# Optimization experiments

Hardware: AMD Instinct MI355X
Metric: run time of the kernel (lower is better)

Reference implementation:

```python
import jax, jax.numpy as jnp
import numpy as np

N, E, D, B = 50000, 800000, 64, 64
NEXP, NC, EDIM, PDIM = 4, 10, 4, 100


def setup_inputs() -> dict:
    key = jax.random.key(0)
    ks = jax.random.split(key, 24)
    s = lambda f: 1.0 / np.sqrt(f)
    inp = {
        'x': jax.random.normal(ks[0], (N, D), jnp.float32),
        'edge_index': jax.random.randint(ks[1], (2, E), 0, N, jnp.int32),
        'edge_attr': jax.random.normal(ks[2], (E, EDIM), jnp.float32),
        'batch': jnp.sort(jax.random.randint(ks[3], (N,), 0, B, jnp.int32)),
        'ldxb_flag': jax.random.normal(ks[4], (B,), jnp.float32),
        # layer 1 params
        'w_edge1': jax.random.normal(ks[5], (D, EDIM)) * s(EDIM),
        'b_edge1': jnp.zeros((D,), jnp.float32),
        'w_ih1': jax.random.normal(ks[6], (3 * D, D)) * s(D),
        'w_hh1': jax.random.normal(ks[7], (3 * D, D)) * s(D),
        'b_ih1': jnp.zeros((3 * D,), jnp.float32),
        'b_hh1': jnp.zeros((3 * D,), jnp.float32),
        # layer 2 params
        'w_edge2': jax.random.normal(ks[8], (D, EDIM)) * s(EDIM),
        'b_edge2': jnp.zeros((D,), jnp.float32),
        'w_ih2': jax.random.normal(ks[9], (3 * D, D)) * s(D),
        'w_hh2': jax.random.normal(ks[10], (3 * D, D)) * s(D),
        'b_ih2': jnp.zeros((3 * D,), jnp.float32),
        'b_hh2': jnp.zeros((3 * D,), jnp.float32),
        # MoE
        'gate_w': jax.random.normal(ks[11], (NEXP, D)) * s(D),
        'gate_b': jnp.zeros((NEXP,), jnp.float32),
        'exp_w': jax.random.normal(ks[12], (NEXP, D, D)) * s(D),
        'exp_b': jnp.zeros((NEXP, D), jnp.float32),
        # heads
        'proj_w': jax.random.normal(ks[13], (PDIM, 1)),
        'proj_b': jnp.zeros((PDIM,), jnp.float32),
        'fc_w': jax.random.normal(ks[14], (NC, D + PDIM)) * s(D + PDIM),
        'fc_b': jnp.zeros((NC,), jnp.float32),
    }
    return inp


def _ggnn_layer(x, src, dst, eemb, w_ih, w_hh, b_ih, b_hh):
    # gather + scatter-add message passing (self-loops already in src/dst/eemb)
    msg = x[src] + eemb                       # [E+N, D]
    m = jnp.zeros_like(x).at[dst].add(msg)    # [N, D]
    # GRUCell(m, x): x is the hidden state
    gi = m @ w_ih.T + b_ih
    gh = x @ w_hh.T + b_hh
    i_r, i_z, i_n = jnp.split(gi, 3, axis=1)
    h_r, h_z, h_n = jnp.split(gh, 3, axis=1)
    r = jax.nn.sigmoid(i_r + h_r)
    z = jax.nn.sigmoid(i_z + h_z)
    n = jnp.tanh(i_n + r * h_n)
    return (1.0 - z) * n + z * x


def reference(x, edge_index, edge_attr, batch, ldxb_flag,
              w_edge1, b_edge1, w_ih1, w_hh1, b_ih1, b_hh1,
              w_edge2, b_edge2, w_ih2, w_hh2, b_ih2, b_hh2,
              gate_w, gate_b, exp_w, exp_b, proj_w, proj_b, fc_w, fc_b):
    n = x.shape[0]
    loop = jnp.arange(n, dtype=edge_index.dtype)
    src = jnp.concatenate([edge_index[0], loop])
    dst = jnp.concatenate([edge_index[1], loop])
    ea = jnp.concatenate([edge_attr, jnp.zeros((n, edge_attr.shape[1]), edge_attr.dtype)], axis=0)

    h = _ggnn_layer(x, src, dst, ea @ w_edge1.T + b_edge1, w_ih1, w_hh1, b_ih1, b_hh1)
    h = jax.nn.relu(h)
    h = _ggnn_layer(h, src, dst, ea @ w_edge2.T + b_edge2, w_ih2, w_hh2, b_ih2, b_hh2)
    h = jax.nn.relu(h)

    # soft MoE combine
    gw = jax.nn.softmax(h @ gate_w.T + gate_b, axis=1)            # [N, NEXP]
    eo = jax.nn.relu(jnp.einsum('nd,ehd->neh', h, exp_w) + exp_b)  # [N, NEXP, D]
    h = jnp.einsum('ne,neh->nh', gw, eo)                           # [N, D]

    # global mean pool per graph
    sums = jax.ops.segment_sum(h, batch, num_segments=B)
    cnts = jax.ops.segment_sum(jnp.ones((n,), h.dtype), batch, num_segments=B)
    graph_emb = sums / jnp.maximum(cnts, 1.0)[:, None]             # [B, D]

    flag = ldxb_flag[:, None] @ proj_w.T + proj_b                  # [B, 100]
    logits = jnp.concatenate([flag, graph_emb], axis=1) @ fc_w.T + fc_b
    return (graph_emb, graph_emb, logits)
```

## Files before the change

kernel.cpp:

```cpp
#include <hip/hip_runtime.h>
#include <hip/hip_fp16.h>
#include <stdint.h>


#define SUBCAP 8
#define OVF_MAX 32768
#define PS 16

typedef __bf16 bf16x8 __attribute__((ext_vector_type(8)));
typedef float floatx4 __attribute__((ext_vector_type(4)));
typedef unsigned short us8 __attribute__((ext_vector_type(8)));

__device__ __forceinline__ unsigned short f2bf(float f){
  union { float f; unsigned u; } c; c.f = f;
  unsigned r = c.u + 0x7FFFu + ((c.u >> 16) & 1u);
  return (unsigned short)(r >> 16);
}
__device__ __forceinline__ float bf2f(unsigned short u){
  union { unsigned u; float f; } c; c.u = ((unsigned)u) << 16; return c.f;
}
__device__ __forceinline__ unsigned short f2h(float f){
  return __half_as_ushort(__float2half(f));
}
__device__ __forceinline__ float h2f(unsigned short u){
  return __half2float(__ushort_as_half(u));
}
__device__ __forceinline__ float sigm(float x){ return 1.f/(1.f + __expf(-x)); }

__global__ void k_init(const float* __restrict__ s0, const float* __restrict__ s1,
                       const float* __restrict__ s2, const float* __restrict__ s3,
                       const float* __restrict__ s4, const float* __restrict__ s5,
                       unsigned short* __restrict__ dst,
                       int* __restrict__ cur, int* __restrict__ ovfcnt, int N8,
                       const float* __restrict__ xin, unsigned short* __restrict__ x16,
                       int nTot){
  int i = blockIdx.x*blockDim.x + threadIdx.x;
  if (i < N8) cur[i] = 0;
  if (i == 0){ ovfcnt[0] = 0; }
  int base = i*8;
  if (base < nTot){
    const float4* xp = (const float4*)(xin + base);
    float4 a = xp[0], b = xp[1];
    us8 t;
    t[0]=f2h(a.x); t[1]=f2h(a.y); t[2]=f2h(a.z); t[3]=f2h(a.w);
    t[4]=f2h(b.x); t[5]=f2h(b.y); t[6]=f2h(b.z); t[7]=f2h(b.w);
    *(us8*)(x16 + base) = t;
  }
  if (i >= 65792) return;
  const float* s; int off;
  if      (i < 12288){ s = s0; off = i; }
  else if (i < 24576){ s = s1; off = i - 12288; }
  else if (i < 36864){ s = s2; off = i - 24576; }
  else if (i < 49152){ s = s3; off = i - 36864; }
  else if (i < 49408){ s = s4; off = i - 49152; }
  else               { s = s5; off = i - 49408; }
  dst[i] = f2bf(s[off]);
}

__global__ void k_bucket(const int* __restrict__ ei, const float* __restrict__ ea,
                         int* __restrict__ cur, int4* __restrict__ bkt,
                         int* __restrict__ ovfcnt, int* __restrict__ ovf,
                         int E, int N){
  unsigned xcc;
  asm volatile("s_getreg_b32 %0, hwreg(HW_REG_XCC_ID)" : "=s"(xcc));
  int sub = (int)(xcc & 7u);
  int base = blockIdx.x*512;
#pragma unroll
  for (int half = 0; half < 2; ++half){
    int e = base + half*256 + threadIdx.x;
    if (e >= E) continue;
    int s = ei[e];
    int d = ei[E + e];
    size_t sb = (size_t)sub*N + d;
    int pos = __hip_atomic_fetch_add(&cur[sb], 1, __ATOMIC_RELAXED,
                                     __HIP_MEMORY_SCOPE_WORKGROUP);
    if (pos < SUBCAP){
      float4 v = *(const float4*)(ea + (size_t)e*4);
      int4 p;
      p.x = s;
      p.y = (int)(((unsigned)f2bf(v.y) << 16) | (unsigned)f2bf(v.x));
      p.z = (int)(((unsigned)f2bf(v.w) << 16) | (unsigned)f2bf(v.z));
      p.w = 0;
      bkt[sb*SUBCAP + pos] = p;
    } else {
      int o = atomicAdd(ovfcnt, 1);
      if (o < OVF_MAX) ovf[o] = e;
    }
  }
}

__global__ void __launch_bounds__(256) k_gather(
    const int* __restrict__ cur, const int4* __restrict__ bkt,
    const float* __restrict__ xin, const unsigned short* __restrict__ x16,
    const float* __restrict__ w_edge, const float* __restrict__ b_edge,
    float* __restrict__ m, int N){
  int n = (int)(((long long)blockIdx.x*blockDim.x + threadIdx.x) >> 6);
  if (n >= N) return;
  int d = threadIdx.x & 63;
  int sub = d >> 3, k = d & 7;
  size_t sb = (size_t)sub*N + n;
  int myc = cur[sb];
  int contrib = (k == 0) ? myc : 0;
#pragma unroll
  for (int off = 1; off < 64; off <<= 1) contrib += __shfl_xor(contrib, off);
  int degAll = contrib;

  bool valid = k < min(myc, SUBCAP);
  int src = 0;
  float esx = 0.f, esy = 0.f, esz = 0.f, esw = 0.f;
  if (valid){
    int4 p = bkt[sb*SUBCAP + k];
    src = p.x;
    esx = bf2f((unsigned short)(p.y & 0xffff));
    esy = bf2f((unsigned short)(((unsigned)p.y) >> 16));
    esz = bf2f((unsigned short)(p.z & 0xffff));
    esw = bf2f((unsigned short)(((unsigned)p.z) >> 16));
  }

  float4 wv = *(const float4*)(w_edge + d*4);
  float acc = xin[(size_t)n*64 + d] + (float)(degAll + 1) * b_edge[d];

  unsigned long long mm = __ballot(valid);
  while (mm){
    float a0=0.f,a1=0.f,a2=0.f,a3=0.f,a4=0.f,a5=0.f,a6=0.f,a7=0.f;
    {
      int l0 = (int)__builtin_ctzll(mm); mm &= mm - 1;
      a0 = h2f(x16[(size_t)__shfl(src, l0)*64 + d]);
      if (mm){
        int l1 = (int)__builtin_ctzll(mm); mm &= mm - 1;
        a1 = h2f(x16[(size_t)__shfl(src, l1)*64 + d]);
        if (mm){
          int l2 = (int)__builtin_ctzll(mm); mm &= mm - 1;
          a2 = h2f(x16[(size_t)__shfl(src, l2)*64 + d]);
          if (mm){
            int l3 = (int)__builtin_ctzll(mm); mm &= mm - 1;
            a3 = h2f(x16[(size_t)__shfl(src, l3)*64 + d]);
            if (mm){
              int l4 = (int)__builtin_ctzll(mm); mm &= mm - 1;
              a4 = h2f(x16[(size_t)__shfl(src, l4)*64 + d]);
              if (mm){
                int l5 = (int)__builtin_ctzll(mm); mm &= mm - 1;
                a5 = h2f(x16[(size_t)__shfl(src, l5)*64 + d]);
                if (mm){
                  int l6 = (int)__builtin_ctzll(mm); mm &= mm - 1;
                  a6 = h2f(x16[(size_t)__shfl(src, l6)*64 + d]);
                  if (mm){
                    int l7 = (int)__builtin_ctzll(mm); mm &= mm - 1;
                    a7 = h2f(x16[(size_t)__shfl(src, l7)*64 + d]);
                  }
                }
              }
            }
          }
        }
      }
    }
    acc += ((a0 + a1) + (a2 + a3)) + ((a4 + a5) + (a6 + a7));
  }

#pragma unroll
  for (int off = 1; off < 64; off <<= 1){
    esx += __shfl_xor(esx, off);
    esy += __shfl_xor(esy, off);
    esz += __shfl_xor(esz, off);
    esw += __shfl_xor(esw, off);
  }
  acc += esx*wv.x + esy*wv.y + esz*wv.z + esw*wv.w;
  m[(size_t)n*64 + d] = acc;
}

__global__ void k_ovf(const int* __restrict__ ei, const float* __restrict__ ea,
                      const float* __restrict__ xin, const float* __restrict__ w_edge,
                      const int* __restrict__ ovf, const int* __restrict__ ovfcnt,
                      float* __restrict__ m, int E){
  int cnt = *ovfcnt; if (cnt > OVF_MAX) cnt = OVF_MAX;
  int nwaves = (gridDim.x * blockDim.x) >> 6;
  int wid = (int)((blockIdx.x*blockDim.x + threadIdx.x) >> 6);
  int d = threadIdx.x & 63;
  for (int k = wid; k < cnt; k += nwaves){
    int e = ovf[k];
    int s = ei[e], dst = ei[E + e];
    float4 v  = *(const float4*)(ea + (size_t)e*4);
    float4 wv = *(const float4*)(w_edge + d*4);
    float msg = xin[(size_t)s*64 + d] + v.x*wv.x + v.y*wv.y + v.z*wv.z + v.w*wv.w;
    atomicAdd(&m[(size_t)dst*64 + d], msg);
  }
}

__global__ void __launch_bounds__(256) k_gru(
    const float* __restrict__ m, const float* x,
    const unsigned short* __restrict__ wih, const unsigned short* __restrict__ whh,
    const float* __restrict__ b_ih, const float* __restrict__ b_hh,
    float* out, unsigned short* h16out, int tiles, int N){
  int tile = blockIdx.x;
  if (tile >= tiles) return;
  int j    = threadIdx.x >> 6;
  int lane = threadIdx.x & 63;
  int col = lane & 15, quad = lane >> 4;
  int na = tile*16 + col; if (na > N-1) na = N-1;

  bf16x8 am[2], ax[2];
#pragma unroll
  for (int ks = 0; ks < 2; ++ks){
    int kb = ks*32 + quad*8;
    const float4* mp = (const float4*)(m + (size_t)na*64 + kb);
    float4 lo = mp[0], hi = mp[1];
    us8 tm;
    tm[0]=f2bf(lo.x); tm[1]=f2bf(lo.y); tm[2]=f2bf(lo.z); tm[3]=f2bf(lo.w);
    tm[4]=f2bf(hi.x); tm[5]=f2bf(hi.y); tm[6]=f2bf(hi.z); tm[7]=f2bf(hi.w);
    am[ks] = __builtin_bit_cast(bf16x8, tm);
    const float4* xp = (const float4*)(x + (size_t)na*64 + kb);
    float4 xlo = xp[0], xhi = xp[1];
    us8 tx;
    tx[0]=f2bf(xlo.x); tx[1]=f2bf(xlo.y); tx[2]=f2bf(xlo.z); tx[3]=f2bf(xlo.w);
    tx[4]=f2bf(xhi.x); tx[5]=f2bf(xhi.y); tx[6]=f2bf(xhi.z); tx[7]=f2bf(xhi.w);
    ax[ks] = __builtin_bit_cast(bf16x8, tx);
  }
  __syncthreads();

  floatx4 ai[3], ah[3];
#pragma unroll
  for (int g = 0; g < 3; ++g){ ai[g] = (floatx4)0.f; ah[g] = (floatx4)0.f; }
#pragma unroll
  for (int g = 0; g < 3; ++g){
    int r = (g*4 + j)*16 + col;
#pragma unroll
    for (int ks = 0; ks < 2; ++ks){
      int kb = ks*32 + quad*8;
      bf16x8 bi = __builtin_bit_cast(bf16x8, *(const us8*)(wih + (size_t)r*64 + kb));
      ai[g] = __builtin_amdgcn_mfma_f32_16x16x32_bf16(am[ks], bi, ai[g], 0,0,0);
      bf16x8 bh = __builtin_bit_cast(bf16x8, *(const us8*)(whh + (size_t)r*64 + kb));
      ah[g] = __builtin_amdgcn_mfma_f32_16x16x32_bf16(ax[ks], bh, ah[g], 0,0,0);
    }
  }

  int d = j*16 + col;
  float bir = b_ih[d],      bhr = b_hh[d];
  float biz = b_ih[64+d],   bhz = b_hh[64+d];
  float bin = b_ih[128+d],  bhn = b_hh[128+d];
#pragma unroll
  for (int rg = 0; rg < 4; ++rg){
    int node = tile*16 + quad*4 + rg;
    if (node >= N) continue;
    float rr = sigm(ai[0][rg] + bir + ah[0][rg] + bhr);
    float zz = sigm(ai[1][rg] + biz + ah[1][rg] + bhz);
    float nn = tanhf(ai[2][rg] + bin + rr*(ah[2][rg] + bhn));
    float xv = x[(size_t)node*64 + d];
    float hv = fmaxf((1.f - zz)*nn + zz*xv, 0.f);
    out[(size_t)node*64 + d] = hv;
    if (h16out) h16out[(size_t)node*64 + d] = f2h(hv);
  }
}

__global__ void __launch_bounds__(256) k_moe(
    const float* __restrict__ h,
    const unsigned short* __restrict__ gate_w, const float* __restrict__ gate_b,
    const unsigned short* __restrict__ exp_w,  const float* __restrict__ exp_b,
    float* __restrict__ v_out, int tiles, int N){
  __shared__ float gsm[16][4];
  __shared__ float vsm[4][16][65];
  int tile = blockIdx.x;
  if (tile >= tiles) return;
  int e    = threadIdx.x >> 6;
  int lane = threadIdx.x & 63;
  int col = lane & 15, quad = lane >> 4;
  int na = tile*16 + col; if (na > N-1) na = N-1;

  bf16x8 a[2];
#pragma unroll
  for (int ks=0; ks<2; ++ks){
    int kb = ks*32 + quad*8;
    const float4* hp = (const float4*)(h + (size_t)na*64 + kb);
    float4 lo = hp[0], hi = hp[1];
    us8 th;
    th[0]=f2bf(lo.x); th[1]=f2bf(lo.y); th[2]=f2bf(lo.z); th[3]=f2bf(lo.w);
    th[4]=f2bf(hi.x); th[5]=f2bf(hi.y); th[6]=f2bf(hi.z); th[7]=f2bf(hi.w);
    a[ks] = __builtin_bit_cast(bf16x8, th);
  }

  if (e == 0){
    floatx4 accg = (floatx4)0.f;
#pragma unroll
    for (int ks=0; ks<2; ++ks){
      int kb = ks*32 + quad*8;
      us8 braw = {0,0,0,0,0,0,0,0};
      if (col < 4) braw = *(const us8*)(gate_w + col*64 + kb);
      accg = __builtin_amdgcn_mfma_f32_16x16x32_bf16(a[ks], __builtin_bit_cast(bf16x8, braw), accg, 0,0,0);
    }
    if (col < 4){
      float gb = gate_b[col];
#pragma unroll
      for (int rg=0;rg<4;++rg) gsm[quad*4+rg][col] = accg[rg] + gb;
    }
  }

  floatx4 acc[4];
#pragma unroll
  for (int nt=0;nt<4;++nt) acc[nt] = (floatx4)0.f;
#pragma unroll
  for (int nt=0;nt<4;++nt)
#pragma unroll
    for (int ks=0;ks<2;++ks){
      int kb = ks*32 + quad*8;
      bf16x8 b = __builtin_bit_cast(bf16x8,
          *(const us8*)(exp_w + ((size_t)e*64 + nt*16 + col)*64 + kb));
      acc[nt] = __builtin_amdgcn_mfma_f32_16x16x32_bf16(a[ks], b, acc[nt], 0,0,0);
    }
  __syncthreads();

#pragma unroll
  for (int rg=0; rg<4; ++rg){
    int nrow = quad*4 + rg;
    float g0=gsm[nrow][0], g1=gsm[nrow][1], g2=gsm[nrow][2], g3=gsm[nrow][3];
    float mx = fmaxf(fmaxf(g0,g1), fmaxf(g2,g3));
    float e0=__expf(g0-mx), e1=__expf(g1-mx), e2=__expf(g2-mx), e3=__expf(g3-mx);
    float we = ((e==0)?e0:(e==1)?e1:(e==2)?e2:e3) / (e0+e1+e2+e3);
#pragma unroll
    for (int nt=0;nt<4;++nt){
      int o = nt*16 + col;
      vsm[e][nrow][o] = we * fmaxf(acc[nt][rg] + exp_b[e*64 + o], 0.f);
    }
  }
  __syncthreads();

  for (int idx = threadIdx.x; idx < 1024; idx += 256){
    int nrow = idx >> 6, o = idx & 63;
    int node = tile*16 + nrow;
    if (node < N)
      v_out[(size_t)node*64 + o] = vsm[0][nrow][o] + vsm[1][nrow][o]
                                 + vsm[2][nrow][o] + vsm[3][nrow][o];
  }
}

__device__ __forceinline__ int lower_bound_i(const int* __restrict__ a, int n, int key){
  int lo = 0, hi = n;
  while (lo < hi){ int mid = (lo + hi) >> 1; if (a[mid] < key) lo = mid + 1; else hi = mid; }
  return lo;
}

__global__ void __launch_bounds__(256) k_pool(
    const float* __restrict__ v, const int* __restrict__ batch, int N,
    float* __restrict__ partial){
  __shared__ float red[4][64];
  int g = blockIdx.x / PS, s = blockIdx.x % PS;
  int t = threadIdx.x, d = t & 63, r = t >> 6;
  int start = lower_bound_i(batch, N, g);
  int end   = lower_bound_i(batch, N, g + 1);
  int len = end - start;
  int per = (len + PS - 1) / PS;
  int s0 = start + s*per;
  int s1 = s0 + per; if (s1 > end) s1 = end;
  float acc = 0.f;
  for (int i = s0 + r; i < s1; i += 4)
    acc += v[(size_t)i*64 + d];
  red[r][d] = acc;
  __syncthreads();
  if (r == 0)
    partial[(size_t)blockIdx.x*64 + d] = red[0][d] + red[1][d] + red[2][d] + red[3][d];
}

__global__ void __launch_bounds__(64) k_head(
    const float* __restrict__ partial, const int* __restrict__ batch, int N, int B,
    const float* __restrict__ ldxb,
    const float* __restrict__ proj_w, const float* __restrict__ proj_b,
    const float* __restrict__ fc_w, const float* __restrict__ fc_b,
    float* __restrict__ out){
  __shared__ float ges[64];
  int b = blockIdx.x, d = threadIdx.x;
  int start = lower_bound_i(batch, N, b);
  int end   = lower_bound_i(batch, N, b + 1);
  float sum = 0.f;
#pragma unroll
  for (int s = 0; s < PS; ++s)
    sum += partial[((size_t)b*PS + s)*64 + d];
  float ge = sum / fmaxf((float)(end - start), 1.f);
  ges[d] = ge;
  out[(size_t)b*64 + d]                = ge;
  out[(size_t)B*64 + (size_t)b*64 + d] = ge;
  __syncthreads();
  if (d < 10){
    float acc = fc_b[d];
    float fl = ldxb[b];
    const float* fr = fc_w + d*164;
    for (int p = 0; p < 100; ++p) acc += (fl*proj_w[p] + proj_b[p]) * fr[p];
    for (int dd = 0; dd < 64; ++dd) acc += ges[dd]*fr[100 + dd];
    out[(size_t)B*128 + (size_t)b*10 + d] = acc;
  }
}

extern "C" void kernel_launch(void* const* d_in, const int* in_sizes, int n_in,
                              void* d_out, int out_size, void* d_ws, size_t ws_size,
                              hipStream_t stream){
  const float* x      = (const float*)d_in[0];
  const int*   ei     = (const int*)d_in[1];
  const float* ea     = (const float*)d_in[2];
  const int*   batch  = (const int*)d_in[3];
  const float* ldxb   = (const float*)d_in[4];
  const float* w_edge1= (const float*)d_in[5];
  const float* b_edge1= (const float*)d_in[6];
  const float* w_ih1  = (const float*)d_in[7];
  const float* w_hh1  = (const float*)d_in[8];
  const float* b_ih1  = (const float*)d_in[9];
  const float* b_hh1  = (const float*)d_in[10];
  const float* w_edge2= (const float*)d_in[11];
  const float* b_edge2= (const float*)d_in[12];
  const float* w_ih2  = (const float*)d_in[13];
  const float* w_hh2  = (const float*)d_in[14];
  const float* b_ih2  = (const float*)d_in[15];
  const float* b_hh2  = (const float*)d_in[16];
  const float* gate_w = (const float*)d_in[17];
  const float* gate_b = (const float*)d_in[18];
  const float* exp_w  = (const float*)d_in[19];
  const float* exp_b  = (const float*)d_in[20];
  const float* proj_w = (const float*)d_in[21];
  const float* proj_b = (const float*)d_in[22];
  const float* fc_w   = (const float*)d_in[23];
  const float* fc_b   = (const float*)d_in[24];
  float* out = (float*)d_out;

  int N = in_sizes[0] / 64;
  int E = in_sizes[1] / 2;
  int B = in_sizes[4];
  int tiles = (N + 15) / 16;
  int nTot = N * 64;

  float*   m       = (float*)d_ws;
  float*   h       = m + (size_t)nTot;
  int4*    bkt     = (int4*)(h + (size_t)nTot);
  int*     cur     = (int*)(bkt + (size_t)nTot);
  int*     ovfcnt  = cur + (size_t)N*8;
  int*     ovf     = ovfcnt + 4;
  unsigned short* wbf = (unsigned short*)(ovf + OVF_MAX);
  float*   partial = (float*)(wbf + 65792);
  unsigned short* x16 = (unsigned short*)(partial + (size_t)B*PS*64);
  unsigned short* h16 = x16 + (size_t)nTot;
  unsigned short* wih1bf = wbf;
  unsigned short* whh1bf = wbf + 12288;
  unsigned short* wih2bf = wbf + 24576;
  unsigned short* whh2bf = wbf + 36864;
  unsigned short* gatebf = wbf + 49152;
  unsigned short* expbf  = wbf + 49408;

  dim3 blk(256);
  int edgeBlocks = (E + 511)/512;
  int nodeWaveBlocks = (N + 3)/4;
  int N8 = N*8;
  int initThreads = N8 > 65792 ? N8 : 65792;
  if (nTot/8 > initThreads) initThreads = nTot/8;
  int initBlocks = (initThreads + 255)/256;

  k_init<<<initBlocks, blk, 0, stream>>>(w_ih1, w_hh1, w_ih2, w_hh2, gate_w, exp_w,
                                         wbf, cur, ovfcnt, N8, x, x16, nTot);
  k_bucket<<<edgeBlocks, blk, 0, stream>>>(ei, ea, cur, bkt, ovfcnt, ovf, E, N);
  k_gather<<<nodeWaveBlocks, blk, 0, stream>>>(cur, bkt, x, x16, w_edge1, b_edge1, m, N);
  k_ovf<<<8, blk, 0, stream>>>(ei, ea, x, w_edge1, ovf, ovfcnt, m, E);
  k_gru<<<tiles, blk, 0, stream>>>(m, x, wih1bf, whh1bf, b_ih1, b_hh1, h, h16, tiles, N);
  k_gather<<<nodeWaveBlocks, blk, 0, stream>>>(cur, bkt, h, h16, w_edge2, b_edge2, m, N);
  k_ovf<<<8, blk, 0, stream>>>(ei, ea, h, w_edge2, ovf, ovfcnt, m, E);
  k_gru<<<tiles, blk, 0, stream>>>(m, h, wih2bf, whh2bf, b_ih2, b_hh2, h, (unsigned short*)nullptr, tiles, N);
  k_moe<<<tiles, blk, 0, stream>>>(h, gatebf, gate_b, expbf, exp_b, m, tiles, N);
  k_pool<<<B*PS, blk, 0, stream>>>(m, batch, N, partial);
  k_head<<<B, 64, 0, stream>>>(partial, batch, N, B, ldxb, proj_w, proj_b, fc_w, fc_b, out);
}
```

Baseline: 353.9 us.

## Fuse gather, overflow fix-up, GRU and MoE into per-tile kernels

Measured after the change: 349.8 us. About the same (-1.1%).

```diff
diff --git a/kernel.cpp b/kernel.cpp
--- a/kernel.cpp
+++ b/kernel.cpp
@@ -89,64 +89,70 @@
   }
 }
 
-__global__ void __launch_bounds__(256) k_gather(
+__device__ __forceinline__ void gather4_ovf(
     const int* __restrict__ cur, const int4* __restrict__ bkt,
     const float* __restrict__ xin, const unsigned short* __restrict__ x16,
     const float* __restrict__ w_edge, const float* __restrict__ b_edge,
-    float* __restrict__ m, int N){
-  int n = (int)(((long long)blockIdx.x*blockDim.x + threadIdx.x) >> 6);
-  if (n >= N) return;
-  int d = threadIdx.x & 63;
+    const int* __restrict__ ei, const float* __restrict__ ea,
+    const int* __restrict__ ovf, int cnt, int E,
+    float (*mt)[68], int tile, int w, int lane, int N){
+  int d = lane;
   int sub = d >> 3, k = d & 7;
-  size_t sb = (size_t)sub*N + n;
-  int myc = cur[sb];
-  int contrib = (k == 0) ? myc : 0;
-#pragma unroll
-  for (int off = 1; off < 64; off <<= 1) contrib += __shfl_xor(contrib, off);
-  int degAll = contrib;
-
-  bool valid = k < min(myc, SUBCAP);
-  int src = 0;
-  float esx = 0.f, esy = 0.f, esz = 0.f, esw = 0.f;
-  if (valid){
-    int4 p = bkt[sb*SUBCAP + k];
-    src = p.x;
-    esx = bf2f((unsigned short)(p.y & 0xffff));
-    esy = bf2f((unsigned short)(((unsigned)p.y) >> 16));
-    esz = bf2f((unsigned short)(p.z & 0xffff));
-    esw = bf2f((unsigned short)(((unsigned)p.z) >> 16));
-  }
-
   float4 wv = *(const float4*)(w_edge + d*4);
-  float acc = xin[(size_t)n*64 + d] + (float)(degAll + 1) * b_edge[d];
-
-  unsigned long long mm = __ballot(valid);
-  while (mm){
-    float a0=0.f,a1=0.f,a2=0.f,a3=0.f,a4=0.f,a5=0.f,a6=0.f,a7=0.f;
-    {
-      int l0 = (int)__builtin_ctzll(mm); mm &= mm - 1;
-      a0 = h2f(x16[(size_t)__shfl(src, l0)*64 + d]);
-      if (mm){
-        int l1 = (int)__builtin_ctzll(mm); mm &= mm - 1;
-        a1 = h2f(x16[(size_t)__shfl(src, l1)*64 + d]);
+  float be = b_edge[d];
+#pragma unroll
+  for (int nl = 0; nl < 4; ++nl){
+    int row = w*4 + nl;
+    int n = tile*16 + row;
+    if (n >= N){ mt[row][d] = 0.f; continue; }
+    size_t sb = (size_t)sub*N + n;
+    int myc = cur[sb];
+    int contrib = (k == 0) ? myc : 0;
+#pragma unroll
+    for (int off = 1; off < 64; off <<= 1) contrib += __shfl_xor(contrib, off);
+    int degAll = contrib;
+
+    bool valid = k < min(myc, SUBCAP);
+    int src = 0;
+    float esx = 0.f, esy = 0.f, esz = 0.f, esw = 0.f;
+    if (valid){
+      int4 p = bkt[sb*SUBCAP + k];
+      src = p.x;
+      esx = bf2f((unsigned short)(p.y & 0xffff));
+      esy = bf2f((unsigned short)(((unsigned)p.y) >> 16));
+      esz = bf2f((unsigned short)(p.z & 0xffff));
+      esw = bf2f((unsigned short)(((unsigned)p.z) >> 16));
+    }
+    float acc = xin[(size_t)n*64 + d] + (float)(degAll + 1) * be;
+
+    unsigned long long mm = __ballot(valid);
+    while (mm){
+      float a0=0.f,a1=0.f,a2=0.f,a3=0.f,a4=0.f,a5=0.f,a6=0.f,a7=0.f;
+      {
+        int l0 = (int)__builtin_ctzll(mm); mm &= mm - 1;
+        a0 = h2f(x16[(size_t)__shfl(src, l0)*64 + d]);
         if (mm){
-          int l2 = (int)__builtin_ctzll(mm); mm &= mm - 1;
-          a2 = h2f(x16[(size_t)__shfl(src, l2)*64 + d]);
+          int l1 = (int)__builtin_ctzll(mm); mm &= mm - 1;
+          a1 = h2f(x16[(size_t)__shfl(src, l1)*64 + d]);
           if (mm){
-            int l3 = (int)__builtin_ctzll(mm); mm &= mm - 1;
-            a3 = h2f(x16[(size_t)__shfl(src, l3)*64 + d]);
+            int l2 = (int)__builtin_ctzll(mm); mm &= mm - 1;
+            a2 = h2f(x16[(size_t)__shfl(src, l2)*64 + d]);
             if (mm){
-              int l4 = (int)__builtin_ctzll(mm); mm &= mm - 1;
-              a4 = h2f(x16[(size_t)__shfl(src, l4)*64 + d]);
+              int l3 = (int)__builtin_ctzll(mm); mm &= mm - 1;
+              a3 = h2f(x16[(size_t)__shfl(src, l3)*64 + d]);
               if (mm){
-                int l5 = (int)__builtin_ctzll(mm); mm &= mm - 1;
-                a5 = h2f(x16[(size_t)__shfl(src, l5)*64 + d]);
+                int l4 = (int)__builtin_ctzll(mm); mm &= mm - 1;
+                a4 = h2f(x16[(size_t)__shfl(src, l4)*64 + d]);
                 if (mm){
-                  int l6 = (int)__builtin_ctzll(mm); mm &= mm - 1;
-                  a6 = h2f(x16[(size_t)__shfl(src, l6)*64 + d]);
+                  int l5 = (int)__builtin_ctzll(mm); mm &= mm - 1;
+                  a5 = h2f(x16[(size_t)__shfl(src, l5)*64 + d]);
                   if (mm){
-                    int l7 = (int)__builtin_ctzll(mm); mm &= mm - 1;
-                    a7 = h2f(x16[(size_t)__shfl(src, l7)*64 + d]);
+                    int l6 = (int)__builtin_ctzll(mm); mm &= mm - 1;
+                    a6 = h2f(x16[(size_t)__shfl(src, l6)*64 + d]);
+                    if (mm){
+                      int l7 = (int)__builtin_ctzll(mm); mm &= mm - 1;
+                      a7 = h2f(x16[(size_t)__shfl(src, l7)*64 + d]);
+                    }
                   }
                 }
               }
@@ -154,57 +160,50 @@
           }
         }
       }
-    }
-    acc += ((a0 + a1) + (a2 + a3)) + ((a4 + a5) + (a6 + a7));
-  }
-
-#pragma unroll
-  for (int off = 1; off < 64; off <<= 1){
-    esx += __shfl_xor(esx, off);
-    esy += __shfl_xor(esy, off);
-    esz += __shfl_xor(esz, off);
-    esw += __shfl_xor(esw, off);
-  }
-  acc += esx*wv.x + esy*wv.y + esz*wv.z + esw*wv.w;
-  m[(size_t)n*64 + d] = acc;
-}
-
-__global__ void k_ovf(const int* __restrict__ ei, const float* __restrict__ ea,
-                      const float* __restrict__ xin, const float* __restrict__ w_edge,
-                      const int* __restrict__ ovf, const int* __restrict__ ovfcnt,
-                      float* __restrict__ m, int E){
-  int cnt = *ovfcnt; if (cnt > OVF_MAX) cnt = OVF_MAX;
-  int nwaves = (gridDim.x * blockDim.x) >> 6;
-  int wid = (int)((blockIdx.x*blockDim.x + threadIdx.x) >> 6);
-  int d = threadIdx.x & 63;
-  for (int k = wid; k < cnt; k += nwaves){
-    int e = ovf[k];
-    int s = ei[e], dst = ei[E + e];
-    float4 v  = *(const float4*)(ea + (size_t)e*4);
-    float4 wv = *(const float4*)(w_edge + d*4);
-    float msg = xin[(size_t)s*64 + d] + v.x*wv.x + v.y*wv.y + v.z*wv.z + v.w*wv.w;
-    atomicAdd(&m[(size_t)dst*64 + d], msg);
-  }
-}
-
-__global__ void __launch_bounds__(256) k_gru(
-    const float* __restrict__ m, const float* x,
+      acc += ((a0 + a1) + (a2 + a3)) + ((a4 + a5) + (a6 + a7));
+    }
+#pragma unroll
+    for (int off = 1; off < 64; off <<= 1){
+      esx += __shfl_xor(esx, off);
+      esy += __shfl_xor(esy, off);
+      esz += __shfl_xor(esz, off);
+      esw += __shfl_xor(esw, off);
+    }
+    acc += esx*wv.x + esy*wv.y + esz*wv.z + esw*wv.w;
+    mt[row][d] = acc;
+  }
+  int lo = tile*16;
+  for (int base = 0; base < cnt; base += 64){
+    int idx = base + lane;
+    int eid = (idx < cnt) ? ovf[idx] : -1;
+    int dst = (eid >= 0) ? ei[(size_t)E + eid] : -1;
+    int rel = dst - lo;
+    bool hit = (eid >= 0) && (rel >= 0) && (rel < 16) && ((rel >> 2) == w);
+    unsigned long long hm = __ballot(hit);
+    while (hm){
+      int l = (int)__builtin_ctzll(hm); hm &= hm - 1;
+      int e2 = __shfl(eid, l);
+      int r2 = __shfl(rel, l);
+      int s2 = ei[e2];
+      float4 v = *(const float4*)(ea + (size_t)e2*4);
+      float addv = xin[(size_t)s2*64 + d] + v.x*wv.x + v.y*wv.y + v.z*wv.z + v.w*wv.w;
+      mt[r2][d] += addv;
+    }
+  }
+}
+
+__device__ __forceinline__ void gru3(
+    const float (*mt)[68], const float* __restrict__ x,
     const unsigned short* __restrict__ wih, const unsigned short* __restrict__ whh,
-    const float* __restrict__ b_ih, const float* __restrict__ b_hh,
-    float* out, unsigned short* h16out, int tiles, int N){
-  int tile = blockIdx.x;
-  if (tile >= tiles) return;
-  int j    = threadIdx.x >> 6;
-  int lane = threadIdx.x & 63;
-  int col = lane & 15, quad = lane >> 4;
+    int tile, int j, int col, int quad, int N,
+    floatx4* ai, floatx4* ah){
   int na = tile*16 + col; if (na > N-1) na = N-1;
-
   bf16x8 am[2], ax[2];
 #pragma unroll
   for (int ks = 0; ks < 2; ++ks){
     int kb = ks*32 + quad*8;
-    const float4* mp = (const float4*)(m + (size_t)na*64 + kb);
-    float4 lo = mp[0], hi = mp[1];
+    const float* mrow = &mt[col][kb];
+    float4 lo = *(const float4*)mrow, hi = *(const float4*)(mrow + 4);
     us8 tm;
     tm[0]=f2bf(lo.x); tm[1]=f2bf(lo.y); tm[2]=f2bf(lo.z); tm[3]=f2bf(lo.w);
     tm[4]=f2bf(hi.x); tm[5]=f2bf(hi.y); tm[6]=f2bf(hi.z); tm[7]=f2bf(hi.w);
@@ -216,9 +215,6 @@
     tx[4]=f2bf(xhi.x); tx[5]=f2bf(xhi.y); tx[6]=f2bf(xhi.z); tx[7]=f2bf(xhi.w);
     ax[ks] = __builtin_bit_cast(bf16x8, tx);
   }
-  __syncthreads();
-
-  floatx4 ai[3], ah[3];
 #pragma unroll
   for (int g = 0; g < 3; ++g){ ai[g] = (floatx4)0.f; ah[g] = (floatx4)0.f; }
 #pragma unroll
@@ -233,11 +229,34 @@
       ah[g] = __builtin_amdgcn_mfma_f32_16x16x32_bf16(ax[ks], bh, ah[g], 0,0,0);
     }
   }
-
-  int d = j*16 + col;
-  float bir = b_ih[d],      bhr = b_hh[d];
-  float biz = b_ih[64+d],   bhz = b_hh[64+d];
-  float bin = b_ih[128+d],  bhn = b_hh[128+d];
+}
+
+__global__ void __launch_bounds__(256) k_fused1(
+    const int* __restrict__ cur, const int4* __restrict__ bkt,
+    const float* __restrict__ x, const unsigned short* __restrict__ x16,
+    const float* __restrict__ w_edge, const float* __restrict__ b_edge,
+    const int* __restrict__ ei, const float* __restrict__ ea,
+    const int* __restrict__ ovf, const int* __restrict__ ovfcnt, int E,
+    const unsigned short* __restrict__ wih, const unsigned short* __restrict__ whh,
+    const float* __restrict__ b_ih, const float* __restrict__ b_hh,
+    float* __restrict__ hout, unsigned short* __restrict__ h16out,
+    int tiles, int N){
+  __shared__ __align__(16) float mt[16][68];
+  int tile = blockIdx.x; if (tile >= tiles) return;
+  int w = threadIdx.x >> 6, lane = threadIdx.x & 63;
+  int cnt = *ovfcnt; if (cnt > OVF_MAX) cnt = OVF_MAX;
+  gather4_ovf(cur, bkt, x, x16, w_edge, b_edge, ei, ea, ovf, cnt, E,
+              mt, tile, w, lane, N);
+  __syncthreads();
+
+  int col = lane & 15, quad = lane >> 4, j = w;
+  floatx4 ai[3], ah[3];
+  gru3(mt, x, wih, whh, tile, j, col, quad, N, ai, ah);
+
+  int dd = j*16 + col;
+  float bir = b_ih[dd],      bhr = b_hh[dd];
+  float biz = b_ih[64+dd],   bhz = b_hh[64+dd];
+  float bin = b_ih[128+dd],  bhn = b_hh[128+dd];
 #pragma unroll
   for (int rg = 0; rg < 4; ++rg){
     int node = tile*16 + quad*4 + rg;
@@ -245,80 +264,106 @@
     float rr = sigm(ai[0][rg] + bir + ah[0][rg] + bhr);
     float zz = sigm(ai[1][rg] + biz + ah[1][rg] + bhz);
     float nn = tanhf(ai[2][rg] + bin + rr*(ah[2][rg] + bhn));
-    float xv = x[(size_t)node*64 + d];
+    float xv = x[(size_t)node*64 + dd];
     float hv = fmaxf((1.f - zz)*nn + zz*xv, 0.f);
-    out[(size_t)node*64 + d] = hv;
-    if (h16out) h16out[(size_t)node*64 + d] = f2h(hv);
-  }
-}
-
-__global__ void __launch_bounds__(256) k_moe(
-    const float* __restrict__ h,
+    hout[(size_t)node*64 + dd] = hv;
+    h16out[(size_t)node*64 + dd] = f2h(hv);
+  }
+}
+
+__global__ void __launch_bounds__(256) k_fused2(
+    const int* __restrict__ cur, const int4* __restrict__ bkt,
+    const float* __restrict__ h, const unsigned short* __restrict__ h16,
+    const float* __restrict__ w_edge, const float* __restrict__ b_edge,
+    const int* __restrict__ ei, const float* __restrict__ ea,
+    const int* __restrict__ ovf, const int* __restrict__ ovfcnt, int E,
+    const unsigned short* __restrict__ wih, const unsigned short* __restrict__ whh,
+    const float* __restrict__ b_ih, const float* __restrict__ b_hh,
     const unsigned short* __restrict__ gate_w, const float* __restrict__ gate_b,
     const unsigned short* __restrict__ exp_w,  const float* __restrict__ exp_b,
     float* __restrict__ v_out, int tiles, int N){
+  __shared__ __align__(16) float mt[16][68];
+  __shared__ __align__(16) unsigned short ht16s[1024];
   __shared__ float gsm[16][4];
   __shared__ float vsm[4][16][65];
-  int tile = blockIdx.x;
-  if (tile >= tiles) return;
-  int e    = threadIdx.x >> 6;
-  int lane = threadIdx.x & 63;
-  int col = lane & 15, quad = lane >> 4;
-  int na = tile*16 + col; if (na > N-1) na = N-1;
-
-  bf16x8 a[2];
-#pragma unroll
-  for (int ks=0; ks<2; ++ks){
-    int kb = ks*32 + quad*8;
-    const float4* hp = (const float4*)(h + (size_t)na*64 + kb);
-    float4 lo = hp[0], hi = hp[1];
-    us8 th;
-    th[0]=f2bf(lo.x); th[1]=f2bf(lo.y); th[2]=f2bf(lo.z); th[3]=f2bf(lo.w);
-    th[4]=f2bf(hi.x); th[5]=f2bf(hi.y); th[6]=f2bf(hi.z); th[7]=f2bf(hi.w);
-    a[ks] = __builtin_bit_cast(bf16x8, th);
-  }
-
-  if (e == 0){
+  int tile = blockIdx.x; if (tile >= tiles) return;
+  int w = threadIdx.x >> 6, lane = threadIdx.x & 63;
+  int cnt = *ovfcnt; if (cnt > OVF_MAX) cnt = OVF_MAX;
+  gather4_ovf(cur, bkt, h, h16, w_edge, b_edge, ei, ea, ovf, cnt, E,
+              mt, tile, w, lane, N);
+  __syncthreads();
+
+  int col = lane & 15, quad = lane >> 4, j = w;
+  floatx4 ai[3], ah[3];
+  gru3(mt, h, wih, whh, tile, j, col, quad, N, ai, ah);
+
+  int dd = j*16 + col;
+  {
+    float bir = b_ih[dd],      bhr = b_hh[dd];
+    float biz = b_ih[64+dd],   bhz = b_hh[64+dd];
+    float bin = b_ih[128+dd],  bhn = b_hh[128+dd];
+#pragma unroll
+    for (int rg = 0; rg < 4; ++rg){
+      int nloc = quad*4 + rg;
+      int node = tile*16 + nloc;
+      int na2 = node < N ? node : N-1;
+      float rr = sigm(ai[0][rg] + bir + ah[0][rg] + bhr);
+      float zz = sigm(ai[1][rg] + biz + ah[1][rg] + bhz);
+      float nn = tanhf(ai[2][rg] + bin + rr*(ah[2][rg] + bhn));
+      float xv = h[(size_t)na2*64 + dd];
+      float hv = fmaxf((1.f - zz)*nn + zz*xv, 0.f);
+      int addr = (nloc*128 + dd*2) ^ ((nloc & 7) << 4);
+      *(unsigned short*)((char*)ht16s + addr) = f2bf(hv);
+    }
+  }
+  __syncthreads();
+
+  bf16x8 a2[2];
+#pragma unroll
+  for (int ks = 0; ks < 2; ++ks){
+    int badd = (col*128 + ks*64 + quad*16) ^ ((col & 7) << 4);
+    a2[ks] = __builtin_bit_cast(bf16x8, *(const us8*)((const char*)ht16s + badd));
+  }
+  if (j == 0){
     floatx4 accg = (floatx4)0.f;
 #pragma unroll
-    for (int ks=0; ks<2; ++ks){
+    for (int ks = 0; ks < 2; ++ks){
       int kb = ks*32 + quad*8;
       us8 braw = {0,0,0,0,0,0,0,0};
       if (col < 4) braw = *(const us8*)(gate_w + col*64 + kb);
-      accg = __builtin_amdgcn_mfma_f32_16x16x32_bf16(a[ks], __builtin_bit_cast(bf16x8, braw), accg, 0,0,0);
+      accg = __builtin_amdgcn_mfma_f32_16x16x32_bf16(a2[ks], __builtin_bit_cast(bf16x8, braw), accg, 0,0,0);
     }
     if (col < 4){
       float gb = gate_b[col];
 #pragma unroll
-      for (int rg=0;rg<4;++rg) gsm[quad*4+rg][col] = accg[rg] + gb;
-    }
-  }
-
-  floatx4 acc[4];
-#pragma unroll
-  for (int nt=0;nt<4;++nt) acc[nt] = (floatx4)0.f;
-#pragma unroll
-  for (int nt=0;nt<4;++nt)
-#pragma unroll
-    for (int ks=0;ks<2;++ks){
+      for (int rg = 0; rg < 4; ++rg) gsm[quad*4+rg][col] = accg[rg] + gb;
+    }
+  }
+  floatx4 acc2[4];
+#pragma unroll
+  for (int nt = 0; nt < 4; ++nt) acc2[nt] = (floatx4)0.f;
+#pragma unroll
+  for (int nt = 0; nt < 4; ++nt)
+#pragma unroll
+    for (int ks = 0; ks < 2; ++ks){
       int kb = ks*32 + quad*8;
       bf16x8 b = __builtin_bit_cast(bf16x8,
-          *(const us8*)(exp_w + ((size_t)e*64 + nt*16 + col)*64 + kb));
-      acc[nt] = __builtin_amdgcn_mfma_f32_16x16x32_bf16(a[ks], b, acc[nt], 0,0,0);
-    }
-  __syncthreads();
-
-#pragma unroll
-  for (int rg=0; rg<4; ++rg){
+          *(const us8*)(exp_w + ((size_t)j*64 + nt*16 + col)*64 + kb));
+      acc2[nt] = __builtin_amdgcn_mfma_f32_16x16x32_bf16(a2[ks], b, acc2[nt], 0,0,0);
+    }
+  __syncthreads();
+
+#pragma unroll
+  for (int rg = 0; rg < 4; ++rg){
     int nrow = quad*4 + rg;
     float g0=gsm[nrow][0], g1=gsm[nrow][1], g2=gsm[nrow][2], g3=gsm[nrow][3];
     float mx = fmaxf(fmaxf(g0,g1), fmaxf(g2,g3));
     float e0=__expf(g0-mx), e1=__expf(g1-mx), e2=__expf(g2-mx), e3=__expf(g3-mx);
-    float we = ((e==0)?e0:(e==1)?e1:(e==2)?e2:e3) / (e0+e1+e2+e3);
-#pragma unroll
-    for (int nt=0;nt<4;++nt){
+    float we = ((j==0)?e0:(j==1)?e1:(j==2)?e2:e3) / (e0+e1+e2+e3);
+#pragma unroll
+    for (int nt = 0; nt < 4; ++nt){
       int o = nt*16 + col;
-      vsm[e][nrow][o] = we * fmaxf(acc[nt][rg] + exp_b[e*64 + o], 0.f);
+      vsm[j][nrow][o] = we * fmaxf(acc2[nt][rg] + exp_b[j*64 + o], 0.f);
     }
   }
   __syncthreads();
@@ -424,8 +469,8 @@
   int tiles = (N + 15) / 16;
   int nTot = N * 64;
 
-  float*   m       = (float*)d_ws;
-  float*   h       = m + (size_t)nTot;
+  float*   v       = (float*)d_ws;
+  float*   h       = v + (size_t)nTot;
   int4*    bkt     = (int4*)(h + (size_t)nTot);
   int*     cur     = (int*)(bkt + (size_t)nTot);
   int*     ovfcnt  = cur + (size_t)N*8;
@@ -443,7 +488,6 @@
 
   dim3 blk(256);
   int edgeBlocks = (E + 511)/512;
-  int nodeWaveBlocks = (N + 3)/4;
   int N8 = N*8;
   int initThreads = N8 > 65792 ? N8 : 65792;
   if (nTot/8 > initThreads) initThreads = nTot/8;
@@ -452,13 +496,15 @@
   k_init<<<initBlocks, blk, 0, stream>>>(w_ih1, w_hh1, w_ih2, w_hh2, gate_w, exp_w,
                                          wbf, cur, ovfcnt, N8, x, x16, nTot);
   k_bucket<<<edgeBlocks, blk, 0, stream>>>(ei, ea, cur, bkt, ovfcnt, ovf, E, N);
-  k_gather<<<nodeWaveBlocks, blk, 0, stream>>>(cur, bkt, x, x16, w_edge1, b_edge1, m, N);
-  k_ovf<<<8, blk, 0, stream>>>(ei, ea, x, w_edge1, ovf, ovfcnt, m, E);
-  k_gru<<<tiles, blk, 0, stream>>>(m, x, wih1bf, whh1bf, b_ih1, b_hh1, h, h16, tiles, N);
-  k_gather<<<nodeWaveBlocks, blk, 0, stream>>>(cur, bkt, h, h16, w_edge2, b_edge2, m, N);
-  k_ovf<<<8, blk, 0, stream>>>(ei, ea, h, w_edge2, ovf, ovfcnt, m, E);
-  k_gru<<<tiles, blk, 0, stream>>>(m, h, wih2bf, whh2bf, b_ih2, b_hh2, h, (unsigned short*)nullptr, tiles, N);
-  k_moe<<<tiles, blk, 0, stream>>>(h, gatebf, gate_b, expbf, exp_b, m, tiles, N);
-  k_pool<<<B*PS, blk, 0, stream>>>(m, batch, N, partial);
+  k_fused1<<<tiles, blk, 0, stream>>>(cur, bkt, x, x16, w_edge1, b_edge1,
+                                      ei, ea, ovf, ovfcnt, E,
+                                      wih1bf, whh1bf, b_ih1, b_hh1,
+                                      h, h16, tiles, N);
+  k_fused2<<<tiles, blk, 0, stream>>>(cur, bkt, h, h16, w_edge2, b_edge2,
+                                      ei, ea, ovf, ovfcnt, E,
+                                      wih2bf, whh2bf, b_ih2, b_hh2,
+                                      gatebf, gate_b, expbf, exp_b,
+                                      v, tiles, N);
+  k_pool<<<B*PS, blk, 0, stream>>>(v, batch, N, partial);
   k_head<<<B, 64, 0, stream>>>(partial, batch, N, B, ldxb, proj_w, proj_b, fc_w, fc_b, out);
 }
```
